# Kernel optimization log

Hardware: AMD Instinct MI355X
Metric: run time of the kernel (lower is better)

The kernel has to match this reference:

```python
import jax, jax.numpy as jnp
import numpy as np

B, T, H, W, P = 2, 4, 224, 224, 16
D, DI, NS, RK, KC = 768, 1536, 16, 48, 4
DEPTH = 16
NV, NA = 196, 24                 # video/audio patches per frame
NTOT = (NV + 2 + NA + 2) * T     # 896 tokens (cls + patches + global, both modalities)
LVIS = NTOT // 2                 # 448 visible tokens


def setup_inputs():
    key = jax.random.key(0)
    ks = iter(jax.random.split(key, 64))
    def nrm(shape, s=0.02):
        return jax.random.normal(next(ks), shape, jnp.float32) * s
    inp = {}
    inp['x_v'] = jax.random.normal(next(ks), (B, 3, T, H, W), jnp.float32)
    inp['x_a'] = jax.random.normal(next(ks), (B, 64, 96 * T), jnp.float32)
    inp['patch_v_w'] = nrm((D, 3, P, P)); inp['patch_v_b'] = jnp.zeros((D,), jnp.float32)
    inp['patch_a_w'] = nrm((D, 1, P, P)); inp['patch_a_b'] = jnp.zeros((D,), jnp.float32)
    inp['pos_v'] = nrm((1, NV, D)); inp['pos_a'] = nrm((1, NA, D))
    inp['tpos_v'] = nrm((1, T, D)); inp['tpos_a'] = nrm((1, T, D))
    inp['cls_v'] = nrm((1, 1, D)); inp['cls_a'] = nrm((1, 1, D))
    inp['glob_v'] = nrm((1, 1, D)); inp['glob_a'] = nrm((1, 1, D))
    inp['norm_w'] = jnp.ones((DEPTH, D), jnp.float32)
    inp['in_w'] = nrm((DEPTH, 2 * DI, D))
    inp['conv_w'] = nrm((DEPTH, DI, KC), 0.2); inp['conv_b'] = jnp.zeros((DEPTH, DI), jnp.float32)
    inp['conv_w_b'] = nrm((DEPTH, DI, KC), 0.2); inp['conv_b_b'] = jnp.zeros((DEPTH, DI), jnp.float32)
    inp['xproj_w'] = nrm((DEPTH, RK + 2 * NS, DI))
    inp['xproj_w_b'] = nrm((DEPTH, RK + 2 * NS, DI))
    inp['dt_w'] = nrm((DEPTH, DI, RK), 0.1)
    inp['dt_w_b'] = nrm((DEPTH, DI, RK), 0.1)
    # mamba dt-bias init: inverse-softplus of dt ~ logU[1e-3, 0.1]
    lo, hi = np.log(1e-3), np.log(0.1)
    u = jax.random.uniform(next(ks), (DEPTH, DI), jnp.float32)
    dt = jnp.exp(u * (hi - lo) + lo)
    inp['dt_b'] = dt + jnp.log(-jnp.expm1(-dt))
    u2 = jax.random.uniform(next(ks), (DEPTH, DI), jnp.float32)
    dt2 = jnp.exp(u2 * (hi - lo) + lo)
    inp['dt_b_b'] = dt2 + jnp.log(-jnp.expm1(-dt2))
    alog = jnp.log(jnp.arange(1, NS + 1, dtype=jnp.float32))  # S4D-real init
    inp['A_log'] = jnp.broadcast_to(alog, (DEPTH, DI, NS)) + 0.0
    inp['A_log_b'] = jnp.broadcast_to(alog, (DEPTH, DI, NS)) + 0.0
    inp['D_par'] = jnp.ones((DEPTH, DI), jnp.float32)
    inp['D_par_b'] = jnp.ones((DEPTH, DI), jnp.float32)
    inp['out_w'] = nrm((DEPTH, D, DI))
    rng = np.random.default_rng(0)
    vi = np.stack([np.sort(rng.choice(NTOT, LVIS, replace=False)) for _ in range(B)])
    inp['vis_idx'] = jnp.asarray(vi, jnp.int32)
    return inp


def _causal_conv1d(x, w, b):
    # x: [B,L,DI]; depthwise causal conv, kernel KC
    xt = x.transpose(0, 2, 1)
    y = jax.lax.conv_general_dilated(xt, w[:, None, :], (1,), [(KC - 1, 0)], feature_group_count=DI)
    return (y + b[None, :, None]).transpose(0, 2, 1)


def _ssd(xc, dt, Bm, Cm, A, Dp):
    # selective scan: xc,dt [B,L,DI]; Bm,Cm [B,L,NS]; A [DI,NS]
    dA = jnp.exp(dt[..., None] * A)                         # B,L,DI,NS
    dBx = dt[..., None] * Bm[:, :, None, :] * xc[..., None]
    def step(h, s):
        a, bx, c = s
        h = a * h + bx
        return h, jnp.einsum('bdn,bn->bd', h, c)
    h0 = jnp.zeros((xc.shape[0], DI, NS), xc.dtype)
    _, ys = jax.lax.scan(step, h0, (jnp.swapaxes(dA, 0, 1), jnp.swapaxes(dBx, 0, 1), jnp.swapaxes(Cm, 0, 1)))
    return jnp.swapaxes(ys, 0, 1) + xc * Dp


def _mamba_dir(xi, zi, cw, cb, xw, dw, db, alog, dp):
    xc = jax.nn.silu(_causal_conv1d(xi, cw, cb))
    proj = jnp.einsum('bld,ed->ble', xc, xw)
    dtr, Bm, Cm = jnp.split(proj, [RK, RK + NS], axis=-1)
    dt = jax.nn.softplus(jnp.einsum('blr,dr->bld', dtr, dw) + db)
    y = _ssd(xc, dt, Bm, Cm, -jnp.exp(alog), dp)
    return y * jax.nn.silu(zi)


def reference(x_v, x_a, patch_v_w, patch_v_b, patch_a_w, patch_a_b, pos_v, pos_a, tpos_v, tpos_a,
              cls_v, cls_a, glob_v, glob_a, norm_w, in_w, conv_w, conv_b, conv_w_b, conv_b_b,
              xproj_w, xproj_w_b, dt_w, dt_b, dt_w_b, dt_b_b, A_log, A_log_b, D_par, D_par_b,
              out_w, vis_idx):
    Bn = x_v.shape[0]
    # video patch embed: conv3d k=(1,16,16) as unfold + matmul
    xv = x_v.transpose(0, 2, 3, 4, 1).reshape(Bn, T, H // P, P, W // P, P, 3)
    xv = xv.transpose(0, 1, 2, 4, 3, 5, 6).reshape(Bn, T, NV, P * P * 3)
    wv = patch_v_w.transpose(0, 2, 3, 1).reshape(D, -1)   # (kh,kw,c) flattening order
    xv = xv @ wv.T + patch_v_b                            # B,T,196,D
    # audio patch embed: [B,64,TA] -> [B,1,TA,64] conv2d 16x16
    TA = x_a.shape[-1]
    xa = x_a.transpose(0, 2, 1).reshape(Bn, TA // P, P, 64 // P, P)
    xa = xa.transpose(0, 1, 3, 2, 4).reshape(Bn, (TA // P) * (64 // P), P * P)
    xa = xa @ patch_a_w.reshape(D, -1).T + patch_a_b      # B, T*24, D
    xa = xa.reshape(Bn, T, NA, D)
    # spatial + temporal positional embeddings
    xv = xv + pos_v[None] + tpos_v[:, :, None, :]
    xa = xa + pos_a[None] + tpos_a[:, :, None, :]
    def add_tokens(x, cls, glob):
        BT = x.shape[0]
        return jnp.concatenate([jnp.broadcast_to(cls, (BT, 1, D)), x, jnp.broadcast_to(glob, (BT, 1, D))], 1)
    xv = add_tokens(xv.reshape(Bn * T, NV, D), cls_v, glob_v).reshape(Bn, T, NV + 2, D)
    xa = add_tokens(xa.reshape(Bn * T, NA, D), cls_a, glob_a).reshape(Bn, T, NA + 2, D)
    x = jnp.concatenate([xv, xa], 2).reshape(Bn, -1, D)   # B, 896, D
    x_vis = jnp.take_along_axis(x, vis_idx[:, :, None], axis=1)  # B, 448, D (x[~mask])

    def layer(carry, p):
        h, res = carry
        nw, iw, cw, cb, cwb, cbb, xw, xwb, dw, db, dwb, dbb, al, alb, dp, dpb, ow = p
        res = h + res                                     # fused add (drop_path=identity at eval)
        hn = res * jax.lax.rsqrt(jnp.mean(res * res, -1, keepdims=True) + 1e-5) * nw  # RMSNorm
        xz = jnp.einsum('bld,ed->ble', hn, iw)
        xi, zi = jnp.split(xz, 2, axis=-1)
        yf = _mamba_dir(xi, zi, cw, cb, xw, dw, db, al, dp)
        yb = _mamba_dir(xi[:, ::-1], zi[:, ::-1], cwb, cbb, xwb, dwb, dbb, alb, dpb)
        h = jnp.einsum('bld,ed->ble', yf + yb[:, ::-1], ow)
        return (h, res), None

    carry = (x_vis, jnp.zeros_like(x_vis))
    (h, res), _ = jax.lax.scan(layer, carry, (norm_w, in_w, conv_w, conv_b, conv_w_b, conv_b_b,
                                              xproj_w, xproj_w_b, dt_w, dt_b, dt_w_b, dt_b_b,
                                              A_log, A_log_b, D_par, D_par_b, out_w))
    # clip_return_layer=1 -> return_index=[depth-1]; only the post-loop append of the
    # final residual fires, so forward_features returns stack([residual]) of shape [1,B,L,D]
    return res[None]
```

## Files before the change

### kernel.cpp

```cpp
#include <hip/hip_runtime.h>
#include <math.h>

typedef unsigned short ushort_t;
typedef __attribute__((ext_vector_type(8))) short bf16x8;
typedef __attribute__((ext_vector_type(4))) float f32x4;
typedef __attribute__((ext_vector_type(4))) unsigned short us4;
typedef __attribute__((ext_vector_type(8))) unsigned short us8;

#define NBATCH 2
#define TT 4
#define DD 768
#define DI_ 1536
#define NS_ 16
#define RK_ 48
#define KC_ 4
#define DEPTH_ 16
#define NRUN 15
#define LV 448
#define NROWS (NBATCH*LV)
#define NCH 7
#define CLEN 64

#define WIN_SZ   (NRUN*2359296)
#define WOUT_SZ  (NRUN*1179648)
#define WX_SZ    (NRUN*2*196608)
#define WALL_USH (WIN_SZ + WOUT_SZ + WX_SZ)

#define ABUF 2048
#define BBUF 4096

__device__ __forceinline__ float silu_f(float x) { return x / (1.f + __expf(-x)); }
__device__ __forceinline__ ushort_t f2bf(float x) {
  unsigned int u = __float_as_uint(x);
  return (ushort_t)((u + 0x7FFFu + ((u >> 16) & 1u)) >> 16);
}
__device__ __forceinline__ float bf2f(ushort_t h) {
  return __uint_as_float(((unsigned int)h) << 16);
}

typedef const __attribute__((address_space(1))) unsigned int* gas1_t;
typedef __attribute__((address_space(3))) unsigned int* las3_t;
__device__ __forceinline__ void gll16(const ushort_t* g, ushort_t* l) {
  __builtin_amdgcn_global_load_lds((gas1_t)g, (las3_t)l, 16, 0, 0);
}

__global__ __launch_bounds__(256) void mfma_gemm(
    const ushort_t* __restrict__ A, const ushort_t* __restrict__ A2, int lda,
    const ushort_t* __restrict__ W, const ushort_t* __restrict__ W2, int ldw,
    const float* __restrict__ bias, const float* __restrict__ bias2,
    float* __restrict__ C, float* __restrict__ C2, int ldc,
    int M, int K, int nkChunks, long partStride, int epi)
{
  int z = blockIdx.z;
  int dir = z / nkChunks, chunk = z - dir * nkChunks;
  if (dir) { A = A2; W = W2; C = C2; bias = bias2; }
  int kChunk = K / nkChunks;
  int kbeg = chunk * kChunk;
  if (nkChunks > 1) C += (long)chunk * partStride;

  __shared__ __align__(16) ushort_t At[3 * ABUF];
  __shared__ __align__(16) ushort_t Bt[3 * BBUF];

  int tid = threadIdx.x, wv = tid >> 6, lane = tid & 63;
  int m0 = blockIdx.y * 64, n0 = blockIdx.x * 128;

  int rA = tid >> 2, gA = (tid & 3) ^ ((rA >> 1) & 3);
  const ushort_t* aSrc = A + (size_t)min(m0 + rA, M - 1) * lda + gA * 8 + kbeg;
  int aOff = tid * 8;
  int SB0 = tid, SB1 = tid + 256;
  int rB0 = SB0 >> 2, gB0 = (SB0 & 3) ^ ((rB0 >> 1) & 3);
  int rB1 = SB1 >> 2, gB1 = (SB1 & 3) ^ ((rB1 >> 1) & 3);
  const ushort_t* bSrc0 = W + (size_t)(n0 + rB0) * ldw + gB0 * 8 + kbeg;
  const ushort_t* bSrc1 = W + (size_t)(n0 + rB1) * ldw + gB1 * 8 + kbeg;
  int bOff0 = SB0 * 8, bOff1 = SB1 * 8;

  int wr = wv >> 1, wc = wv & 1;
  int rl = lane & 15, gl = lane >> 4;
  int offA[2], offB[4];
#pragma unroll
  for (int i = 0; i < 2; ++i) {
    int ra = wr * 32 + i * 16 + rl;
    offA[i] = ra * 32 + ((gl ^ ((ra >> 1) & 3)) * 8);
  }
#pragma unroll
  for (int j = 0; j < 4; ++j) {
    int rb = wc * 64 + j * 16 + rl;
    offB[j] = rb * 32 + ((gl ^ ((rb >> 1) & 3)) * 8);
  }

  f32x4 acc[2][4] = {};
  int nk = kChunk >> 5;
  gll16(aSrc, At + aOff);
  gll16(bSrc0, Bt + bOff0);
  gll16(bSrc1, Bt + bOff1);
  if (nk > 1) {
    gll16(aSrc + 32, At + ABUF + aOff);
    gll16(bSrc0 + 32, Bt + BBUF + bOff0);
    gll16(bSrc1 + 32, Bt + BBUF + bOff1);
  }
  int bufT = 0;
  for (int t = 0; t < nk; ++t) {
    int bufN = bufT + 2; if (bufN >= 3) bufN -= 3;
    if (t + 2 < nk) {
      int ko = (t + 2) << 5;
      gll16(aSrc + ko, At + bufN * ABUF + aOff);
      gll16(bSrc0 + ko, Bt + bufN * BBUF + bOff0);
      gll16(bSrc1 + ko, Bt + bufN * BBUF + bOff1);
      asm volatile("s_waitcnt vmcnt(6)" ::: "memory");
    } else if (t + 1 < nk) {
      asm volatile("s_waitcnt vmcnt(3)" ::: "memory");
    } else {
      asm volatile("s_waitcnt vmcnt(0)" ::: "memory");
    }
    __builtin_amdgcn_s_barrier();
    __builtin_amdgcn_sched_barrier(0);
    const ushort_t* Ab = At + bufT * ABUF;
    const ushort_t* Bb = Bt + bufT * BBUF;
    bf16x8 af[2], bw[4];
#pragma unroll
    for (int i = 0; i < 2; ++i) af[i] = *(const bf16x8*)(Ab + offA[i]);
#pragma unroll
    for (int j = 0; j < 4; ++j) bw[j] = *(const bf16x8*)(Bb + offB[j]);
#pragma unroll
    for (int i = 0; i < 2; ++i)
#pragma unroll
      for (int j = 0; j < 4; ++j)
        acc[i][j] = __builtin_amdgcn_mfma_f32_16x16x32_bf16(af[i], bw[j], acc[i][j], 0, 0, 0);
    asm volatile("s_waitcnt lgkmcnt(0)" ::: "memory");
    __builtin_amdgcn_s_barrier();
    __builtin_amdgcn_sched_barrier(0);
    bufT += 1; if (bufT == 3) bufT = 0;
  }

#pragma unroll
  for (int i = 0; i < 2; ++i) {
    int row0 = m0 + wr * 32 + i * 16 + gl * 4;
#pragma unroll
    for (int q = 0; q < 4; ++q) {
      int row = row0 + q;
      if (row >= M) continue;
#pragma unroll
      for (int j = 0; j < 4; ++j) {
        int col = n0 + wc * 64 + j * 16 + rl;
        float v = acc[i][j][q];
        if (bias) v += bias[col];
        if (epi & 1) v = (v > 20.f) ? v : log1pf(__expf(v));
        if (epi & 2) ((ushort_t*)C)[(size_t)row * ldc + col] = f2bf(v);
        else C[(size_t)row * ldc + col] = v;
      }
    }
  }
}

__global__ __launch_bounds__(256) void cast4_k(const float* __restrict__ s, ushort_t* __restrict__ d, int n4)
{
  int i = blockIdx.x * 256 + threadIdx.x;
  if (i >= n4) return;
  f32x4 v = *(const f32x4*)(s + i * 4);
  us4 o = { f2bf(v[0]), f2bf(v[1]), f2bf(v[2]), f2bf(v[3]) };
  *(us4*)(d + i * 4) = o;
}

__global__ __launch_bounds__(256) void cast8_k(const float* __restrict__ s, ushort_t* __restrict__ d, int n8)
{
  int i = blockIdx.x * 256 + threadIdx.x;
  if (i >= n8) return;
  f32x4 v0 = *(const f32x4*)(s + i * 8);
  f32x4 v1 = *(const f32x4*)(s + i * 8 + 4);
  us8 o = { f2bf(v0[0]), f2bf(v0[1]), f2bf(v0[2]), f2bf(v0[3]),
            f2bf(v1[0]), f2bf(v1[1]), f2bf(v1[2]), f2bf(v1[3]) };
  *(us8*)(d + i * 8) = o;
}

__global__ __launch_bounds__(256) void castx8_k(
    const float* __restrict__ xw0, const float* __restrict__ xwb0,
    ushort_t* __restrict__ WX, int nl)
{
  int i = blockIdx.x * 256 + threadIdx.x;
  if (i >= nl * 2 * 24576) return;
  int ld = i / 24576;
  int j = (i - ld * 24576) * 8;
  int l = ld >> 1;
  const float* xs = ((ld & 1) ? xwb0 : xw0) + (size_t)l * 122880;
  int r = j / 1536, k = j - r * 1536;
  f32x4 v0 = {0.f,0.f,0.f,0.f}, v1 = {0.f,0.f,0.f,0.f};
  if (r < 80) { v0 = *(const f32x4*)(xs + r * 1536 + k); v1 = *(const f32x4*)(xs + r * 1536 + k + 4); }
  us8 o = { f2bf(v0[0]), f2bf(v0[1]), f2bf(v0[2]), f2bf(v0[3]),
            f2bf(v1[0]), f2bf(v1[1]), f2bf(v1[2]), f2bf(v1[3]) };
  *(us8*)(WX + (size_t)ld * 196608 + j) = o;
}

__global__ __launch_bounds__(256) void im2col_v(const float* __restrict__ xv, ushort_t* __restrict__ Av)
{
  int i = blockIdx.x * 256 + threadIdx.x;
  if (i >= 1568 * 768) return;
  int m = i / 768, k = i % 768;
  int c = k >> 8, r = k & 255;
  int kh = r >> 4, kw = r & 15;
  int bt = m / 196, n = m % 196;
  int b = bt / TT, t = bt % TT;
  int hb = n / 14, wb = n % 14;
  Av[i] = f2bf(xv[(size_t)b * 602112 + (size_t)c * 200704 + t * 50176 + (hb * 16 + kh) * 224 + wb * 16 + kw]);
}

__global__ __launch_bounds__(256) void im2col_a(const float* __restrict__ xa, ushort_t* __restrict__ Aa)
{
  int i = blockIdx.x * 256 + threadIdx.x;
  if (i >= 192 * 256) return;
  int m = i / 256, k = i % 256;
  int kh = k >> 4, kw = k & 15;
  int b = m / 96, q = m % 96;
  int tb = q >> 2, fb = q & 3;
  Aa[i] = f2bf(xa[(size_t)b * 24576 + (fb * 16 + kw) * 384 + tb * 16 + kh]);
}

__global__ __launch_bounds__(256) void assemble_k(
    const float* __restrict__ tokv, const float* __restrict__ toka,
    const float* __restrict__ pos_v, const float* __restrict__ pos_a,
    const float* __restrict__ tpos_v, const float* __restrict__ tpos_a,
    const float* __restrict__ cls_v, const float* __restrict__ cls_a,
    const float* __restrict__ glob_v, const float* __restrict__ glob_a,
    const int* __restrict__ vis_idx,
    float* __restrict__ h, float* __restrict__ res)
{
  int i = blockIdx.x * 256 + threadIdx.x;
  if (i >= NROWS * DD) return;
  int d = i % DD;
  int bl = i / DD;
  int r = bl % LV, b = bl / LV;
  int tok = vis_idx[b * LV + r];
  int t = tok / 224, q = tok % 224;
  float v;
  if (q == 0) v = cls_v[d];
  else if (q <= 196) {
    int n = q - 1;
    v = tokv[((size_t)(b * TT + t) * 196 + n) * DD + d] + pos_v[n * DD + d] + tpos_v[t * DD + d];
  } else if (q == 197) v = glob_v[d];
  else if (q == 198) v = cls_a[d];
  else if (q <= 222) {
    int n = q - 199;
    v = toka[((size_t)b * 96 + t * 24 + n) * DD + d] + pos_a[n * DD + d] + tpos_a[t * DD + d];
  } else v = glob_a[d];
  h[i] = v;
  res[i] = 0.f;
}

__global__ __launch_bounds__(256) void rmsnorm_k(
    const float* __restrict__ hsrc, const float* __restrict__ part,
    float* __restrict__ res, ushort_t* __restrict__ hn, const float* __restrict__ nw)
{
  int row = blockIdx.x;
  float* rp = res + (size_t)row * DD;
  ushort_t* op = hn + (size_t)row * DD;
  int tid = threadIdx.x;
  float v[3];
  float ss = 0.f;
#pragma unroll
  for (int i = 0; i < 3; ++i) {
    int c = tid + i * 256;
    float x;
    if (part) {
      x = part[(size_t)row * DD + c] + part[688128 + (size_t)row * DD + c]
        + part[2 * 688128 + (size_t)row * DD + c] + part[3 * 688128 + (size_t)row * DD + c];
    } else {
      x = hsrc[(size_t)row * DD + c];
    }
    x += rp[c];
    v[i] = x;
    ss += x * x;
  }
  for (int m = 1; m < 64; m <<= 1) ss += __shfl_xor(ss, m, 64);
  __shared__ float sred[4];
  if ((tid & 63) == 0) sred[tid >> 6] = ss;
  __syncthreads();
  float tot = sred[0] + sred[1] + sred[2] + sred[3];
  float sc = rsqrtf(tot / (float)DD + 1e-5f);
#pragma unroll
  for (int i = 0; i < 3; ++i) {
    int c = tid + i * 256;
    rp[c] = v[i];
    op[c] = f2bf(v[i] * sc * nw[c]);
  }
}

__global__ __launch_bounds__(256) void conv_k(
    const ushort_t* __restrict__ xz,
    const float* __restrict__ cw, const float* __restrict__ cb,
    const float* __restrict__ cwb, const float* __restrict__ cbb,
    ushort_t* __restrict__ xcFb, ushort_t* __restrict__ xcBb)
{
  int i = blockIdx.x * 256 + threadIdx.x;
  if (i >= NROWS * (DI_ / 4)) return;
  int dv = (i % (DI_ / 4)) * 4;
  int bl = i / (DI_ / 4);
  int l = bl % LV, b = bl / LV;
  const ushort_t* xzb = xz + (size_t)b * LV * (2 * DI_);
  f32x4 accf = *(const f32x4*)(cb + dv);
  f32x4 accb = *(const f32x4*)(cbb + dv);
  f32x4 tf[4], tb[4];
#pragma unroll
  for (int e = 0; e < 4; ++e) {
    tf[e] = *(const f32x4*)(cw + (dv + e) * 4);
    tb[e] = *(const f32x4*)(cwb + (dv + e) * 4);
  }
#pragma unroll
  for (int j = 0; j < 4; ++j) {
    int lp = l - 3 + j;
    if (lp >= 0) {
      us4 xf = *(const us4*)(xzb + (size_t)lp * (2 * DI_) + dv);
      us4 xb = *(const us4*)(xzb + (size_t)(LV - 1 - lp) * (2 * DI_) + dv);
#pragma unroll
      for (int e = 0; e < 4; ++e) {
        accf[e] += bf2f(xf[e]) * tf[e][j];
        accb[e] += bf2f(xb[e]) * tb[e][j];
      }
    }
  }
  us4 of, ob;
#pragma unroll
  for (int e = 0; e < 4; ++e) {
    of[e] = f2bf(silu_f(accf[e]));
    ob[e] = f2bf(silu_f(accb[e]));
  }
  *(us4*)(xcFb + (size_t)bl * DI_ + dv) = of;
  *(us4*)(xcBb + (size_t)bl * DI_ + dv) = ob;
}

__global__ __launch_bounds__(256) void reddt_k(
    const float* __restrict__ pF, const float* __restrict__ pB,
    float* __restrict__ prF, float* __restrict__ prB,
    const float* __restrict__ dwF, const float* __restrict__ dwB,
    const float* __restrict__ dbF, const float* __restrict__ dbB,
    ushort_t* __restrict__ dtFb, ushort_t* __restrict__ dtBb)
{
  int dir = blockIdx.y;
  const float* part = dir ? pB : pF;
  float* proj = dir ? prB : prF;
  const float* dw = dir ? dwB : dwF;
  const float* db = dir ? dbB : dbF;
  ushort_t* dt = dir ? dtBb : dtFb;
  int r0 = blockIdx.x * 8;
  int tid = threadIdx.x;
  __shared__ float sdtr[8][48];
  for (int o = tid; o < 8 * 80; o += 256) {
    int r = o / 80, col = o - (o / 80) * 80;
    int row = r0 + r;
    float s = 0.f;
#pragma unroll
    for (int c = 0; c < 8; ++c) s += part[c * (NROWS * 128) + row * 128 + col];
    proj[row * 80 + col] = s;
    if (col < 48) sdtr[r][col] = s;
  }
  __syncthreads();
#pragma unroll
  for (int q = 0; q < 6; ++q) {
    int d = q * 256 + tid;
    f32x4 w[12];
#pragma unroll
    for (int e = 0; e < 12; ++e) w[e] = *(const f32x4*)(dw + (size_t)d * 48 + e * 4);
    float bias = db[d];
#pragma unroll
    for (int r = 0; r < 8; ++r) {
      float s = bias;
#pragma unroll
      for (int e = 0; e < 12; ++e) {
#pragma unroll
        for (int u = 0; u < 4; ++u) s += sdtr[r][e * 4 + u] * w[e][u];
      }
      s = (s > 20.f) ? s : log1pf(__expf(s));
      dt[(size_t)(r0 + r) * DI_ + d] = f2bf(s);
    }
  }
}

__global__ __launch_bounds__(256) void scanA_k(
    const ushort_t* __restrict__ xcFb, const ushort_t* __restrict__ dtF, const float* __restrict__ prF,
    const ushort_t* __restrict__ xcBb, const ushort_t* __restrict__ dtB, const float* __restrict__ prB,
    const float* __restrict__ AlF, const float* __restrict__ AlB,
    float* __restrict__ hloc, float* __restrict__ Pb)
{
  int dir = blockIdx.z;
  const ushort_t* xc = dir ? xcBb : xcFb;
  const ushort_t* dt = dir ? dtB : dtF;
  const float* pr = dir ? prB : prF;
  const float* Al = dir ? AlB : AlF;
  int c = blockIdx.y;
  int g = blockIdx.x * 16 + (threadIdx.x >> 4);
  int n = threadIdx.x & 15;
  int b = g / DI_, d = g % DI_;
  float An = -__expf(Al[d * NS_ + n]);
  const ushort_t* xcp = xc + (size_t)b * LV * DI_ + d;
  const ushort_t* dtp = dt + (size_t)b * LV * DI_ + d;
  const float* prp = pr + (size_t)b * LV * 80;
  int l0 = c * CLEN;
  float hs = 0.f, S = 0.f;
  float dtv = bf2f(dtp[(size_t)l0 * DI_]);
  float xcv = bf2f(xcp[(size_t)l0 * DI_]);
  float bn  = prp[l0 * 80 + 48 + n];
  for (int kk = 0; kk < CLEN; ++kk) {
    float dtv_n = 0.f, xcv_n = 0.f, bn_n = 0.f;
    if (kk < CLEN - 1) {
      int l1 = l0 + kk + 1;
      dtv_n = bf2f(dtp[(size_t)l1 * DI_]);
      xcv_n = bf2f(xcp[(size_t)l1 * DI_]);
      bn_n  = prp[l1 * 80 + 48 + n];
    }
    hs = __expf(dtv * An) * hs + dtv * bn * xcv;
    S += dtv;
    dtv = dtv_n; xcv = xcv_n; bn = bn_n;
  }
  int idx = ((dir * 3072 + g) * 6 + c) * NS_ + n;
  hloc[idx] = hs;
  Pb[idx] = __expf(An * S);
}

__global__ __launch_bounds__(256) void scanBC_k(
    const ushort_t* __restrict__ xcFb, const ushort_t* __restrict__ dtF, const float* __restrict__ prF,
    const ushort_t* __restrict__ xcBb, const ushort_t* __restrict__ dtB, const float* __restrict__ prB,
    const float* __restrict__ AlF, const float* __restrict__ AlB,
    const float* __restrict__ DpF, const float* __restrict__ DpB,
    const float* __restrict__ hloc, const float* __restrict__ Pb,
    const ushort_t* __restrict__ xz, ushort_t* __restrict__ yc)
{
  int c = blockIdx.y;
  int tid = threadIdx.x;
  int n = tid & 15, gi = (tid >> 4) & 7, dir = tid >> 7;
  int g = blockIdx.x * 8 + gi;
  int b = g / DI_, d = g % DI_;
  __shared__ float sbuf[2][8][65];

  const ushort_t* xc = dir ? xcBb : xcFb;
  const ushort_t* dt = dir ? dtB : dtF;
  const float* pr = dir ? prB : prF;
  const float* Al = dir ? AlB : AlF;
  const float* Dpp = dir ? DpB : DpF;
  int myc = dir ? (6 - c) : c;
  float An = -__expf(Al[d * NS_ + n]);
  float Dpd = Dpp[d];
  float hs = 0.f;
  for (int j = 0; j < myc; ++j) {
    int idx = ((dir * 3072 + g) * 6 + j) * NS_ + n;
    hs = Pb[idx] * hs + hloc[idx];
  }
  const ushort_t* xcp = xc + (size_t)b * LV * DI_ + d;
  const ushort_t* dtp = dt + (size_t)b * LV * DI_ + d;
  const float* prp = pr + (size_t)b * LV * 80;
  int l0 = myc * CLEN;
  float dtv = bf2f(dtp[(size_t)l0 * DI_]);
  float xcv = bf2f(xcp[(size_t)l0 * DI_]);
  float bn  = prp[l0 * 80 + 48 + n];
  float cn  = prp[l0 * 80 + 64 + n];
  for (int kk = 0; kk < CLEN; ++kk) {
    float dtv_n = 0.f, xcv_n = 0.f, bn_n = 0.f, cn_n = 0.f;
    if (kk < CLEN - 1) {
      int l1 = l0 + kk + 1;
      dtv_n = bf2f(dtp[(size_t)l1 * DI_]);
      xcv_n = bf2f(xcp[(size_t)l1 * DI_]);
      bn_n  = prp[l1 * 80 + 48 + n];
      cn_n  = prp[l1 * 80 + 64 + n];
    }
    hs = __expf(dtv * An) * hs + dtv * bn * xcv;
    float p = hs * cn;
    p += __shfl_xor(p, 1, 16);
    p += __shfl_xor(p, 2, 16);
    p += __shfl_xor(p, 4, 16);
    p += __shfl_xor(p, 8, 16);
    if (n == 0) {
      int off = dir ? (CLEN - 1 - kk) : kk;
      sbuf[dir][gi][off] = p + xcv * Dpd;
    }
    dtv = dtv_n; xcv = xcv_n; bn = bn_n; cn = cn_n;
  }
  __syncthreads();
  for (int oid = tid; oid < 512; oid += 256) {
    int gi2 = oid & 7, kk = oid >> 3;
    int g2 = blockIdx.x * 8 + gi2;
    int b2 = g2 / DI_, d2 = g2 % DI_;
    int l = c * CLEN + kk;
    float z = bf2f(xz[((size_t)b2 * LV + l) * 3072 + 1536 + d2]);
    float v = (sbuf[0][gi2][kk] + sbuf[1][gi2][kk]) * silu_f(z);
    yc[((size_t)b2 * LV + l) * DI_ + d2] = f2bf(v);
  }
}

__global__ __launch_bounds__(256) void final_k(
    const float* __restrict__ res, const float* __restrict__ part, float* __restrict__ out)
{
  int i = blockIdx.x * 256 + threadIdx.x;
  if (i >= NROWS * DD) return;
  out[i] = res[i] + part[i] + part[688128 + i] + part[2 * 688128 + i] + part[3 * 688128 + i];
}

extern "C" void kernel_launch(void* const* d_in, const int* in_sizes, int n_in,
                              void* d_out, int out_size, void* d_ws, size_t ws_size,
                              hipStream_t stream)
{
  const float* x_v = (const float*)d_in[0];
  const float* x_a = (const float*)d_in[1];
  const float* patch_v_w = (const float*)d_in[2];
  const float* patch_v_b = (const float*)d_in[3];
  const float* patch_a_w = (const float*)d_in[4];
  const float* patch_a_b = (const float*)d_in[5];
  const float* pos_v = (const float*)d_in[6];
  const float* pos_a = (const float*)d_in[7];
  const float* tpos_v = (const float*)d_in[8];
  const float* tpos_a = (const float*)d_in[9];
  const float* cls_v = (const float*)d_in[10];
  const float* cls_a = (const float*)d_in[11];
  const float* glob_v = (const float*)d_in[12];
  const float* glob_a = (const float*)d_in[13];
  const float* norm_w = (const float*)d_in[14];
  const float* in_w = (const float*)d_in[15];
  const float* conv_w = (const float*)d_in[16];
  const float* conv_b = (const float*)d_in[17];
  const float* conv_w_b = (const float*)d_in[18];
  const float* conv_b_b = (const float*)d_in[19];
  const float* xproj_w = (const float*)d_in[20];
  const float* xproj_w_b = (const float*)d_in[21];
  const float *dt_w, *dt_bias, *dt_w_b, *dt_bias_b;
  if (in_sizes[23] == DEPTH_ * DI_ * RK_) {
    dt_w = (const float*)d_in[22]; dt_w_b = (const float*)d_in[23];
    dt_bias = (const float*)d_in[24]; dt_bias_b = (const float*)d_in[25];
  } else {
    dt_w = (const float*)d_in[22]; dt_bias = (const float*)d_in[23];
    dt_w_b = (const float*)d_in[24]; dt_bias_b = (const float*)d_in[25];
  }
  const float* A_log = (const float*)d_in[26];
  const float* A_log_b = (const float*)d_in[27];
  const float* D_par = (const float*)d_in[28];
  const float* D_par_b = (const float*)d_in[29];
  const float* out_w = (const float*)d_in[30];
  const int* vis_idx = (const int*)d_in[31];

  float* ws = (float*)d_ws;
  float* res   = ws;
  float* hbuf  = ws + 688128;
  float* R1    = ws + 1376256;
  float* R2f   = ws + 4128768;
  float* R3    = ws + 4816896;
  float* xz    = ws + 7569408;
  float* dtFf  = ws + 10321920;
  float* dtBf  = ws + 11698176;
  float* projF = ws + 13074432;
  float* projB = ws + 13146112;
  float* wPvf  = ws + 13217792;
  float* WALLf = ws + 13512704;

  float* partF = R1;
  float* partB = R1 + 917504;
  float* hloc  = R1;
  float* Pb    = R1 + 589824;
  float* partO = R1;
  float* tokv  = R1;
  float* toka  = R1 + 1204224;
  ushort_t* Av_bf = (ushort_t*)xz;
  ushort_t* wPv   = (ushort_t*)wPvf;
  ushort_t* wPa   = (ushort_t*)dtFf;
  ushort_t* Aa_bf = ((ushort_t*)dtFf) + 196608;
  ushort_t* hn_bf = (ushort_t*)R2f;
  ushort_t* ycb   = (ushort_t*)R2f;
  ushort_t* xcFb = (ushort_t*)R3;
  ushort_t* xcBb = ((ushort_t*)R3) + 1376256;
  ushort_t* xzb  = (ushort_t*)xz;
  ushort_t* dtFb = (ushort_t*)dtFf;
  ushort_t* dtBb = (ushort_t*)dtBf;

  size_t need_big = ((size_t)13512704 + (WALL_USH + 1) / 2) * 4;
  int bigws = ws_size >= need_big;
  ushort_t* WALL = (ushort_t*)WALLf;
  ushort_t* WIN  = WALL;
  ushort_t* WOUT = WIN + WIN_SZ;
  ushort_t* WX   = WOUT + WOUT_SZ;

  dim3 blk(256);

  if (bigws) {
    cast8_k<<<(WIN_SZ / 8 + 255) / 256, blk, 0, stream>>>(in_w, WIN, WIN_SZ / 8);
    cast8_k<<<(WOUT_SZ / 8 + 255) / 256, blk, 0, stream>>>(out_w, WOUT, WOUT_SZ / 8);
    castx8_k<<<(NRUN * 2 * 24576 + 255) / 256, blk, 0, stream>>>(xproj_w, xproj_w_b, WX, NRUN);
  }

  im2col_v<<<4704, blk, 0, stream>>>(x_v, Av_bf);
  cast4_k<<<576, blk, 0, stream>>>(patch_v_w, wPv, 147456);
  cast4_k<<<192, blk, 0, stream>>>(patch_a_w, wPa, 49152);
  im2col_a<<<192, blk, 0, stream>>>(x_a, Aa_bf);
  mfma_gemm<<<dim3(6, 25, 1), blk, 0, stream>>>(Av_bf, nullptr, 768, wPv, nullptr, 768,
                                                patch_v_b, nullptr, tokv, nullptr, 768,
                                                1568, 768, 1, 0, 0);
  mfma_gemm<<<dim3(6, 3, 1), blk, 0, stream>>>(Aa_bf, nullptr, 256, wPa, nullptr, 256,
                                               patch_a_b, nullptr, toka, nullptr, 768,
                                               192, 256, 1, 0, 0);
  assemble_k<<<2688, blk, 0, stream>>>(tokv, toka, pos_v, pos_a, tpos_v, tpos_a,
                                       cls_v, cls_a, glob_v, glob_a, vis_idx, hbuf, res);

  for (int l = 0; l < NRUN; ++l) {
    const float* nw  = norm_w + l * DD;
    const float* cw  = conv_w + l * DI_ * KC_;
    const float* cb  = conv_b + l * DI_;
    const float* cwb = conv_w_b + l * DI_ * KC_;
    const float* cbb = conv_b_b + l * DI_;
    const float* dwF = dt_w + (size_t)l * DI_ * RK_;
    const float* dwB = dt_w_b + (size_t)l * DI_ * RK_;
    const float* dbi = dt_bias + l * DI_;
    const float* dbib = dt_bias_b + l * DI_;
    const float* al  = A_log + (size_t)l * DI_ * NS_;
    const float* alb = A_log_b + (size_t)l * DI_ * NS_;
    const float* dp  = D_par + l * DI_;
    const float* dpb = D_par_b + l * DI_;

    ushort_t *wIn, *wOut, *wXF, *wXB;
    if (bigws) {
      wIn  = WIN + (size_t)l * 2359296;
      wOut = WOUT + (size_t)l * 1179648;
      wXF  = WX + (size_t)(l * 2) * 196608;
      wXB  = wXF + 196608;
    } else {
      wIn = WALL; wOut = wIn + 2359296; wXF = wOut + 1179648; wXB = wXF + 196608;
      cast8_k<<<(2359296 / 8 + 255) / 256, blk, 0, stream>>>(in_w + (size_t)l * 2359296, wIn, 2359296 / 8);
      cast8_k<<<(1179648 / 8 + 255) / 256, blk, 0, stream>>>(out_w + (size_t)l * 1179648, wOut, 1179648 / 8);
      castx8_k<<<(2 * 24576 + 255) / 256, blk, 0, stream>>>(xproj_w + (size_t)l * 122880,
                                                            xproj_w_b + (size_t)l * 122880, wXF, 1);
    }

    rmsnorm_k<<<NROWS, blk, 0, stream>>>(hbuf, l ? partO : nullptr, res, hn_bf, nw);
    mfma_gemm<<<dim3(24, 14, 1), blk, 0, stream>>>(hn_bf, nullptr, 768, wIn, nullptr, 768,
                                                   nullptr, nullptr, (float*)xzb, nullptr, 3072,
                                                   NROWS, 768, 1, 0, 2);
    conv_k<<<1344, blk, 0, stream>>>(xzb, cw, cb, cwb, cbb, xcFb, xcBb);
    mfma_gemm<<<dim3(1, 14, 16), blk, 0, stream>>>(xcFb, xcBb, 1536, wXF, wXB, 1536,
                                                   nullptr, nullptr, partF, partB, 128,
                                                   NROWS, 1536, 8, NROWS * 128, 0);
    reddt_k<<<dim3(112, 2, 1), blk, 0, stream>>>(partF, partB, projF, projB,
                                                 dwF, dwB, dbi, dbib, dtFb, dtBb);
    scanA_k<<<dim3(192, 6, 2), blk, 0, stream>>>(xcFb, dtFb, projF, xcBb, dtBb, projB,
                                                 al, alb, hloc, Pb);
    scanBC_k<<<dim3(384, NCH, 1), blk, 0, stream>>>(xcFb, dtFb, projF, xcBb, dtBb, projB,
                                                    al, alb, dp, dpb, hloc, Pb, xzb, ycb);
    mfma_gemm<<<dim3(6, 14, 4), blk, 0, stream>>>(ycb, nullptr, 1536, wOut, nullptr, 1536,
                                                  nullptr, nullptr, partO, nullptr, 768,
                                                  NROWS, 1536, 4, NROWS * DD, 0);
  }

  final_k<<<2688, blk, 0, stream>>>(res, partO, (float*)d_out);
}
```

Baseline: 2.544 ms.

## Fuse causal conv, x-projection and dt projection into one per-row kernel

Replaces the conv kernel, the split-K MFMA x-projection GEMM and the partial-reduction/dt kernel with a single kernel. Each block handles four rows: it computes the bidirectional conv+SiLU into shared memory, does the 80-wide x-projection with scalar FP32 dot products, then applies the dt projection and softplus. This removes two launches and the round trip of split-K partial sums through global memory. In exchange the x-projection no longer uses matrix cores, only 160 of 256 threads work in that phase, and each block re-reads the full projection weights.

```diff
diff --git a/kernel.cpp b/kernel.cpp
--- a/kernel.cpp
+++ b/kernel.cpp
@@ -20,6 +20,7 @@
 #define NROWS (NBATCH*LV)
 #define NCH 7
 #define CLEN 64
+#define CPD_ROWS 4
 
 #define WIN_SZ   (NRUN*2359296)
 #define WOUT_SZ  (NRUN*1179648)
@@ -283,92 +284,111 @@
   }
 }
 
-__global__ __launch_bounds__(256) void conv_k(
+__global__ __launch_bounds__(256) void cpd_k(
     const ushort_t* __restrict__ xz,
     const float* __restrict__ cw, const float* __restrict__ cb,
     const float* __restrict__ cwb, const float* __restrict__ cbb,
-    ushort_t* __restrict__ xcFb, ushort_t* __restrict__ xcBb)
-{
-  int i = blockIdx.x * 256 + threadIdx.x;
-  if (i >= NROWS * (DI_ / 4)) return;
-  int dv = (i % (DI_ / 4)) * 4;
-  int bl = i / (DI_ / 4);
-  int l = bl % LV, b = bl / LV;
-  const ushort_t* xzb = xz + (size_t)b * LV * (2 * DI_);
-  f32x4 accf = *(const f32x4*)(cb + dv);
-  f32x4 accb = *(const f32x4*)(cbb + dv);
-  f32x4 tf[4], tb[4];
-#pragma unroll
-  for (int e = 0; e < 4; ++e) {
-    tf[e] = *(const f32x4*)(cw + (dv + e) * 4);
-    tb[e] = *(const f32x4*)(cwb + (dv + e) * 4);
-  }
-#pragma unroll
-  for (int j = 0; j < 4; ++j) {
-    int lp = l - 3 + j;
-    if (lp >= 0) {
-      us4 xf = *(const us4*)(xzb + (size_t)lp * (2 * DI_) + dv);
-      us4 xb = *(const us4*)(xzb + (size_t)(LV - 1 - lp) * (2 * DI_) + dv);
-#pragma unroll
-      for (int e = 0; e < 4; ++e) {
-        accf[e] += bf2f(xf[e]) * tf[e][j];
-        accb[e] += bf2f(xb[e]) * tb[e][j];
-      }
-    }
-  }
-  us4 of, ob;
-#pragma unroll
-  for (int e = 0; e < 4; ++e) {
-    of[e] = f2bf(silu_f(accf[e]));
-    ob[e] = f2bf(silu_f(accb[e]));
-  }
-  *(us4*)(xcFb + (size_t)bl * DI_ + dv) = of;
-  *(us4*)(xcBb + (size_t)bl * DI_ + dv) = ob;
-}
-
-__global__ __launch_bounds__(256) void reddt_k(
-    const float* __restrict__ pF, const float* __restrict__ pB,
-    float* __restrict__ prF, float* __restrict__ prB,
+    const ushort_t* __restrict__ wXF, const ushort_t* __restrict__ wXB,
     const float* __restrict__ dwF, const float* __restrict__ dwB,
     const float* __restrict__ dbF, const float* __restrict__ dbB,
+    ushort_t* __restrict__ xcFb, ushort_t* __restrict__ xcBb,
+    float* __restrict__ projF, float* __restrict__ projB,
     ushort_t* __restrict__ dtFb, ushort_t* __restrict__ dtBb)
 {
-  int dir = blockIdx.y;
-  const float* part = dir ? pB : pF;
-  float* proj = dir ? prB : prF;
-  const float* dw = dir ? dwB : dwF;
-  const float* db = dir ? dbB : dbF;
-  ushort_t* dt = dir ? dtBb : dtFb;
-  int r0 = blockIdx.x * 8;
+  __shared__ float xcs[2][CPD_ROWS][1536];
+  __shared__ float prs[2][CPD_ROWS][80];
   int tid = threadIdx.x;
-  __shared__ float sdtr[8][48];
-  for (int o = tid; o < 8 * 80; o += 256) {
-    int r = o / 80, col = o - (o / 80) * 80;
-    int row = r0 + r;
-    float s = 0.f;
-#pragma unroll
-    for (int c = 0; c < 8; ++c) s += part[c * (NROWS * 128) + row * 128 + col];
-    proj[row * 80 + col] = s;
-    if (col < 48) sdtr[r][col] = s;
+  int r0 = blockIdx.x * CPD_ROWS;
+
+  for (int u = tid; u < CPD_ROWS * 2 * 384; u += 256) {
+    int dv = (u % 384) * 4;
+    int rd = u / 384;
+    int rr = rd >> 1, dir = rd & 1;
+    int row = r0 + rr;
+    int b = row / LV, l = row % LV;
+    const ushort_t* xzb = xz + (size_t)b * LV * 3072;
+    const float* cwp = dir ? cwb : cw;
+    const float* cbp = dir ? cbb : cb;
+    f32x4 acc = *(const f32x4*)(cbp + dv);
+    f32x4 t[4];
+#pragma unroll
+    for (int e = 0; e < 4; ++e) t[e] = *(const f32x4*)(cwp + (dv + e) * 4);
+#pragma unroll
+    for (int j = 0; j < 4; ++j) {
+      int lp = l - 3 + j;
+      if (lp >= 0) {
+        int srow = dir ? (LV - 1 - lp) : lp;
+        us4 x = *(const us4*)(xzb + (size_t)srow * 3072 + dv);
+#pragma unroll
+        for (int e = 0; e < 4; ++e) acc[e] += bf2f(x[e]) * t[e][j];
+      }
+    }
+    us4 o;
+    f32x4 vs;
+#pragma unroll
+    for (int e = 0; e < 4; ++e) { vs[e] = silu_f(acc[e]); o[e] = f2bf(vs[e]); }
+    ushort_t* xcg = dir ? xcBb : xcFb;
+    *(us4*)(xcg + (size_t)row * DI_ + dv) = o;
+    *(f32x4*)&xcs[dir][rr][dv] = vs;
   }
   __syncthreads();
-#pragma unroll
-  for (int q = 0; q < 6; ++q) {
-    int d = q * 256 + tid;
-    f32x4 w[12];
-#pragma unroll
-    for (int e = 0; e < 12; ++e) w[e] = *(const f32x4*)(dw + (size_t)d * 48 + e * 4);
-    float bias = db[d];
-#pragma unroll
-    for (int r = 0; r < 8; ++r) {
-      float s = bias;
-#pragma unroll
-      for (int e = 0; e < 12; ++e) {
-#pragma unroll
-        for (int u = 0; u < 4; ++u) s += sdtr[r][e * 4 + u] * w[e][u];
+
+  if (tid < 160) {
+    int dir = tid / 80, e = tid - dir * 80;
+    const ushort_t* w = (dir ? wXB : wXF) + (size_t)e * DI_;
+    float a0 = 0.f, a1 = 0.f, a2 = 0.f, a3 = 0.f;
+    for (int k = 0; k < DI_; k += 8) {
+      us8 wv = *(const us8*)(w + k);
+      float wf[8];
+#pragma unroll
+      for (int q = 0; q < 8; ++q) wf[q] = bf2f((ushort_t)wv[q]);
+      f32x4 va, vb;
+      va = *(const f32x4*)&xcs[dir][0][k]; vb = *(const f32x4*)&xcs[dir][0][k + 4];
+      a0 += va[0]*wf[0] + va[1]*wf[1] + va[2]*wf[2] + va[3]*wf[3]
+          + vb[0]*wf[4] + vb[1]*wf[5] + vb[2]*wf[6] + vb[3]*wf[7];
+      va = *(const f32x4*)&xcs[dir][1][k]; vb = *(const f32x4*)&xcs[dir][1][k + 4];
+      a1 += va[0]*wf[0] + va[1]*wf[1] + va[2]*wf[2] + va[3]*wf[3]
+          + vb[0]*wf[4] + vb[1]*wf[5] + vb[2]*wf[6] + vb[3]*wf[7];
+      va = *(const f32x4*)&xcs[dir][2][k]; vb = *(const f32x4*)&xcs[dir][2][k + 4];
+      a2 += va[0]*wf[0] + va[1]*wf[1] + va[2]*wf[2] + va[3]*wf[3]
+          + vb[0]*wf[4] + vb[1]*wf[5] + vb[2]*wf[6] + vb[3]*wf[7];
+      va = *(const f32x4*)&xcs[dir][3][k]; vb = *(const f32x4*)&xcs[dir][3][k + 4];
+      a3 += va[0]*wf[0] + va[1]*wf[1] + va[2]*wf[2] + va[3]*wf[3]
+          + vb[0]*wf[4] + vb[1]*wf[5] + vb[2]*wf[6] + vb[3]*wf[7];
+    }
+    prs[dir][0][e] = a0; prs[dir][1][e] = a1; prs[dir][2][e] = a2; prs[dir][3][e] = a3;
+    float* pg = dir ? projB : projF;
+    pg[(size_t)(r0 + 0) * 80 + e] = a0;
+    pg[(size_t)(r0 + 1) * 80 + e] = a1;
+    pg[(size_t)(r0 + 2) * 80 + e] = a2;
+    pg[(size_t)(r0 + 3) * 80 + e] = a3;
+  }
+  __syncthreads();
+
+  {
+    int dir = tid >> 7;
+    int lane = tid & 127;
+    const float* dw = dir ? dwB : dwF;
+    const float* db = dir ? dbB : dbF;
+    ushort_t* dtg = dir ? dtBb : dtFb;
+#pragma unroll
+    for (int dd = 0; dd < 12; ++dd) {
+      int d = dd * 128 + lane;
+      f32x4 w[12];
+#pragma unroll
+      for (int e = 0; e < 12; ++e) w[e] = *(const f32x4*)(dw + (size_t)d * 48 + e * 4);
+      float bias = db[d];
+#pragma unroll
+      for (int r = 0; r < CPD_ROWS; ++r) {
+        float s = bias;
+#pragma unroll
+        for (int e = 0; e < 12; ++e) {
+#pragma unroll
+          for (int u = 0; u < 4; ++u) s += prs[dir][r][e * 4 + u] * w[e][u];
+        }
+        s = (s > 20.f) ? s : log1pf(__expf(s));
+        dtg[(size_t)(r0 + r) * DI_ + d] = f2bf(s);
       }
-      s = (s > 20.f) ? s : log1pf(__expf(s));
-      dt[(size_t)(r0 + r) * DI_ + d] = f2bf(s);
     }
   }
 }
@@ -546,8 +566,6 @@
   float* wPvf  = ws + 13217792;
   float* WALLf = ws + 13512704;
 
-  float* partF = R1;
-  float* partB = R1 + 917504;
   float* hloc  = R1;
   float* Pb    = R1 + 589824;
   float* partO = R1;
@@ -626,12 +644,9 @@
     mfma_gemm<<<dim3(24, 14, 1), blk, 0, stream>>>(hn_bf, nullptr, 768, wIn, nullptr, 768,
                                                    nullptr, nullptr, (float*)xzb, nullptr, 3072,
                                                    NROWS, 768, 1, 0, 2);
-    conv_k<<<1344, blk, 0, stream>>>(xzb, cw, cb, cwb, cbb, xcFb, xcBb);
-    mfma_gemm<<<dim3(1, 14, 16), blk, 0, stream>>>(xcFb, xcBb, 1536, wXF, wXB, 1536,
-                                                   nullptr, nullptr, partF, partB, 128,
-                                                   NROWS, 1536, 8, NROWS * 128, 0);
-    reddt_k<<<dim3(112, 2, 1), blk, 0, stream>>>(partF, partB, projF, projB,
-                                                 dwF, dwB, dbi, dbib, dtFb, dtBb);
+    cpd_k<<<NROWS / CPD_ROWS, blk, 0, stream>>>(xzb, cw, cb, cwb, cbb, wXF, wXB,
+                                                dwF, dwB, dbi, dbib,
+                                                xcFb, xcBb, projF, projB, dtFb, dtBb);
     scanA_k<<<dim3(192, 6, 2), blk, 0, stream>>>(xcFb, dtFb, projF, xcBb, dtBb, projB,
                                                  al, alb, hloc, Pb);
     scanBC_k<<<dim3(384, NCH, 1), blk, 0, stream>>>(xcFb, dtFb, projF, xcBb, dtBb, projB,
```

Result: slower. 2.892 ms (+13.7%).
